# Kernel tuning notes

Hardware: AMD Instinct MI355X
Metric: run time of the kernel (lower is better)

The kernel has to match this reference:

```python
import jax, jax.numpy as jnp
import numpy as np

B, N, DIM, HEADS, NBS = 64, 197, 768, 12, 10
WIN = (14, 14)
HEAD_DIM = DIM // HEADS
SCALE = HEAD_DIM ** -0.5


def _gen_relative_position_index():
    Wh, Ww = WIN
    num_rel = (2 * Wh - 1) * (2 * Ww - 1) + 3
    coords = np.stack(np.meshgrid(np.arange(Wh), np.arange(Ww), indexing='ij')).reshape(2, -1)
    rel = (coords[:, :, None] - coords[:, None, :]).transpose(1, 2, 0).astype(np.int32)
    rel[:, :, 0] += Wh - 1
    rel[:, :, 1] += Ww - 1
    rel[:, :, 0] *= 2 * Ww - 1
    idx = np.zeros((Wh * Ww + 1, Wh * Ww + 1), dtype=np.int32)
    idx[1:, 1:] = rel.sum(-1)
    idx[0, :] = num_rel - 3
    idx[:, 0] = num_rel - 2
    idx[0, 0] = num_rel - 1
    return jnp.asarray(idx)


def setup_inputs() -> dict:
    key = jax.random.key(0)
    ks = jax.random.split(key, 8)
    s = 0.02  # init scale for learned params
    return {
        'x': jax.random.normal(ks[0], (B, N, DIM), jnp.float32),
        'qkv_weight': jax.random.normal(ks[1], (3 * DIM, DIM), jnp.float32) * s,
        'q_bias': jax.random.normal(ks[2], (NBS, DIM), jnp.float32) * s,
        'v_bias': jax.random.normal(ks[3], (NBS, DIM), jnp.float32) * s,
        'rel_table': jax.random.normal(ks[4], (732, HEADS), jnp.float32) * s,
        'proj_weight': jax.random.normal(ks[5], (DIM, DIM), jnp.float32) * s,
        'proj_bias': jax.random.normal(ks[6], (NBS, DIM), jnp.float32) * s,
        'b_idx': jax.random.randint(ks[7], (B,), 0, NBS),
        'rel_index': _gen_relative_position_index(),
    }


def reference(x, qkv_weight, q_bias, v_bias, rel_table, proj_weight, proj_bias, b_idx, rel_index):
    Bb, Nn, C = x.shape
    # QKV projection (no fused bias), then per-sample bitfit bias (k bias is zero)
    qkv = jnp.einsum('bnc,oc->bno', x, qkv_weight)  # [B, N, 3C]
    qb = q_bias[b_idx][:, None]                     # [B, 1, C]
    vb = v_bias[b_idx][:, None]
    qkv_bias = jnp.concatenate([qb, jnp.zeros_like(qb), vb], axis=-1)
    qkv = (qkv + qkv_bias).reshape(Bb, Nn, 3, HEADS, HEAD_DIM).transpose(2, 0, 3, 1, 4)
    q, k, v = qkv[0], qkv[1], qkv[2]                # [B, H, N, d]
    attn = jnp.einsum('bhnd,bhmd->bhnm', q * SCALE, k)
    # gathered relative position bias: [H, N, N]
    rel_bias = rel_table[rel_index.reshape(-1)].reshape(Nn, Nn, HEADS).transpose(2, 0, 1)
    attn = jax.nn.softmax(attn + rel_bias[None], axis=-1)
    out = jnp.einsum('bhnm,bhmd->bhnd', attn, v)
    out = out.transpose(0, 2, 1, 3).reshape(Bb, Nn, -1)
    # output projection with per-sample bitfit bias
    out = jnp.einsum('bnc,oc->bno', out, proj_weight) + proj_bias[b_idx][:, None]
    return out
```

## Files before the change

kernel.cpp:

```cpp
#include <hip/hip_runtime.h>
#include <stdint.h>

#define B_     64
#define N_     197
#define DIM_   768
#define HEADS_ 12
#define HD_    64
#define M_     (B_*N_)
#define K3_    (3*DIM_)
#define NP_    208
#define VSTR_  232
#define SCALE_ 0.125f
#define GK_    768
#define NKT_   24

typedef _Float16 f16x8 __attribute__((ext_vector_type(8)));
typedef _Float16 f16x4 __attribute__((ext_vector_type(4)));
typedef _Float16 f16x2 __attribute__((ext_vector_type(2)));
typedef float    f32x4 __attribute__((ext_vector_type(4)));

__device__ __forceinline__ void gload_lds16(const void* g, void* l) {
    __builtin_amdgcn_global_load_lds(
        (const __attribute__((address_space(1))) uint32_t*)g,
        (__attribute__((address_space(3))) uint32_t*)l, 16, 0, 0);
}

__global__ __launch_bounds__(256) void cvt_f32_f16(const float* __restrict__ s,
                                                   _Float16* __restrict__ d, int n4) {
    int i = blockIdx.x * 256 + threadIdx.x;
    if (i < n4) {
        const float4 v = *(const float4*)(s + (size_t)i * 4);
        f16x4 o;
        o[0] = (_Float16)v.x; o[1] = (_Float16)v.y;
        o[2] = (_Float16)v.z; o[3] = (_Float16)v.w;
        *(f16x4*)(d + (size_t)i * 4) = o;
    }
}

__global__ __launch_bounds__(256) void biasT_pre(const int* __restrict__ rel_index,
                                                 const float* __restrict__ rel_table,
                                                 float* __restrict__ biasT) {
    int t = blockIdx.x * 256 + threadIdx.x;
    if (t < HEADS_ * NP_ * NP_) {
        int h = t / (NP_ * NP_), rem = t - h * (NP_ * NP_);
        int k = rem / NP_, q = rem - k * NP_;
        float v;
        if (k >= N_)      v = -1e30f;
        else if (q >= N_) v = 0.f;
        else              v = rel_table[rel_index[q * N_ + k] * HEADS_ + h];
        biasT[t] = v;
    }
}

template <int MODE>
__global__ __launch_bounds__(512, 2) void gemm_db(
    const _Float16* __restrict__ A, const _Float16* __restrict__ Bw,
    int M, int Nout,
    const float* __restrict__ qb, const float* __restrict__ vb,
    const float* __restrict__ pb, const int* __restrict__ b_idx,
    _Float16* __restrict__ out_h, float* __restrict__ out_f)
{
    __shared__ __align__(16) _Float16 As[3][16 * 512];
    __shared__ __align__(16) _Float16 Bs[3][8 * 512];

    const int tid  = threadIdx.x;
    const int lane = tid & 63, w = tid >> 6;
    const int wm = w >> 1, wn = w & 1;
    const int fr = lane & 15, g = lane >> 4;
    const int gl8 = ((4 * fr + g) ^ (fr >> 1)) * 8;
    const int lx = lane ^ (lane >> 3);
    const int sr = lx >> 2, sc8 = (lx & 3) * 8;

    const int gx = Nout / 128;
    const int gy = (M + 255) / 256;
    const int nwg = gx * gy;
    const int wgid = blockIdx.x + blockIdx.y * gx;
    const int q8 = nwg >> 3, r8 = nwg & 7;
    const int xcd = wgid & 7, lid = wgid >> 3;
    const int nid = (xcd < r8) ? xcd * (q8 + 1) + lid
                               : r8 * (q8 + 1) + (xcd - r8) * q8 + lid;
    const int m0 = (nid / gx) * 256, n0 = (nid % gx) * 128;

    f32x4 acc[4][4];
    #pragma unroll
    for (int i = 0; i < 4; ++i)
        #pragma unroll
        for (int j = 0; j < 4; ++j) acc[i][j] = (f32x4)0.f;

    auto stage = [&](int buf, int kt) {
        #pragma unroll
        for (int iss = 0; iss < 2; ++iss) {
            int grow = m0 + w * 32 + iss * 16 + sr;
            if (grow >= M) grow = M - 1;
            gload_lds16(A + (size_t)grow * GK_ + kt * 32 + sc8,
                        &As[buf][(2 * w + iss) * 512]);
        }
        int brow = n0 + w * 16 + sr;
        gload_lds16(Bw + (size_t)brow * GK_ + kt * 32 + sc8,
                    &Bs[buf][w * 512]);
    };

    stage(0, 0);
    stage(1, 1);

    for (int t = 0; t < NKT_; ++t) {
        if (t + 1 < NKT_) { asm volatile("s_waitcnt vmcnt(3)" ::: "memory"); }
        else              { asm volatile("s_waitcnt vmcnt(0)" ::: "memory"); }
        __builtin_amdgcn_s_barrier();
        __builtin_amdgcn_sched_barrier(0);
        if (t + 2 < NKT_) stage((t + 2) % 3, t + 2);

        const _Float16* Ac = &As[t % 3][0];
        const _Float16* Bc = &Bs[t % 3][0];
        f16x8 av[4], bv[4];
        #pragma unroll
        for (int i = 0; i < 4; ++i)
            av[i] = *(const f16x8*)&Ac[(wm * 4 + i) * 512 + gl8];
        #pragma unroll
        for (int j = 0; j < 4; ++j)
            bv[j] = *(const f16x8*)&Bc[(wn * 4 + j) * 512 + gl8];
        __builtin_amdgcn_s_setprio(1);
        #pragma unroll
        for (int i = 0; i < 4; ++i)
            #pragma unroll
            for (int j = 0; j < 4; ++j)
                acc[i][j] = __builtin_amdgcn_mfma_f32_16x16x32_f16(av[i], bv[j], acc[i][j], 0, 0, 0);
        __builtin_amdgcn_s_setprio(0);
    }

    #pragma unroll
    for (int mi = 0; mi < 4; ++mi) {
        #pragma unroll
        for (int rr = 0; rr < 4; ++rr) {
            const int row = m0 + wm * 64 + mi * 16 + g * 4 + rr;
            if (row < M) {
                const int bi = b_idx[row / N_];
                #pragma unroll
                for (int ni = 0; ni < 4; ++ni) {
                    const int col = n0 + wn * 64 + ni * 16 + fr;
                    float v = acc[mi][ni][rr];
                    if (MODE == 0) {
                        float bias = 0.f;
                        if (col < DIM_) bias = qb[bi * DIM_ + col];
                        else if (col >= 2 * DIM_) bias = vb[bi * DIM_ + (col - 2 * DIM_)];
                        out_h[(size_t)row * Nout + col] = (_Float16)(v + bias);
                    } else {
                        out_f[(size_t)row * Nout + col] = v + pb[bi * DIM_ + col];
                    }
                }
            }
        }
    }
}

__global__ __launch_bounds__(512, 4) void attn_mfma(
    const _Float16* __restrict__ qkv, const float* __restrict__ biasT,
    _Float16* __restrict__ ctx)
{
    __shared__ __align__(16) _Float16 Klds[26 * 512];
    __shared__ __align__(16) _Float16 VT[HD_ * VSTR_];

    const int b = blockIdx.z, h = blockIdx.y, rt = blockIdx.x;
    const int r0 = rt * 128;
    const int tid = threadIdx.x, lane = tid & 63, w = tid >> 6;
    const int fr = lane & 15, g = lane >> 4;
    const int gl8 = ((4 * fr + g) ^ (fr >> 1)) * 8;

    const size_t baseQ = (size_t)b * N_ * K3_ + h * HD_;
    const size_t baseK = baseQ + DIM_;
    const size_t baseV = baseQ + 2 * DIM_;

    {
        const int l = lane ^ (lane >> 3);
        const int cr = l >> 2, cc = (l & 3) * 8;
        for (int c = w; c < 26; c += 8) {
            const int jf = c >> 1, kk = c & 1;
            int grow = jf * 16 + cr; if (grow > N_ - 1) grow = N_ - 1;
            gload_lds16(qkv + baseK + (size_t)grow * K3_ + kk * 32 + cc,
                        &Klds[c * 512]);
        }
    }
    for (int idx = tid; idx < 112 * 8; idx += 512) {
        int jp = idx % 112, dc = idx / 112;
        int j0 = 2 * jp, j1 = 2 * jp + 1;
        f16x8 zz = {};
        f16x8 v0 = (j0 < N_) ? *(const f16x8*)(qkv + baseV + (size_t)j0 * K3_ + dc * 8) : zz;
        f16x8 v1 = (j1 < N_) ? *(const f16x8*)(qkv + baseV + (size_t)j1 * K3_ + dc * 8) : zz;
        #pragma unroll
        for (int e = 0; e < 8; ++e) {
            f16x2 p; p[0] = v0[e]; p[1] = v1[e];
            *(f16x2*)(VT + (dc * 8 + e) * VSTR_ + 2 * jp) = p;
        }
    }
    int qrow = r0 + w * 16 + fr; if (qrow > N_ - 1) qrow = N_ - 1;
    f16x8 qf[2];
    qf[0] = *(const f16x8*)(qkv + baseQ + (size_t)qrow * K3_ + g * 8);
    qf[1] = *(const f16x8*)(qkv + baseQ + (size_t)qrow * K3_ + 32 + g * 8);

    __syncthreads();

    f32x4 p[13];
    #pragma unroll
    for (int jf = 0; jf < 13; ++jf) p[jf] = (f32x4)0.f;
    #pragma unroll
    for (int jf = 0; jf < 13; ++jf) {
        #pragma unroll
        for (int kk = 0; kk < 2; ++kk) {
            f16x8 a = *(const f16x8*)&Klds[(jf * 2 + kk) * 512 + gl8];
            p[jf] = __builtin_amdgcn_mfma_f32_16x16x32_f16(a, qf[kk], p[jf], 0, 0, 0);
        }
    }

    const int qb_ = min(r0 + w * 16 + fr, NP_ - 1);
    const float* bp = biasT + (size_t)h * NP_ * NP_ + qb_;
    float mx = -3e38f;
    #pragma unroll
    for (int jf = 0; jf < 13; ++jf) {
        #pragma unroll
        for (int r = 0; r < 4; ++r) {
            int k = jf * 16 + g * 4 + r;
            float s = p[jf][r] * SCALE_ + bp[(size_t)k * NP_];
            p[jf][r] = s;
            mx = fmaxf(mx, s);
        }
    }
    mx = fmaxf(mx, __shfl_xor(mx, 16));
    mx = fmaxf(mx, __shfl_xor(mx, 32));
    float sum = 0.f;
    #pragma unroll
    for (int jf = 0; jf < 13; ++jf) {
        #pragma unroll
        for (int r = 0; r < 4; ++r) {
            float e = __expf(p[jf][r] - mx);
            p[jf][r] = e;
            sum += e;
        }
    }
    sum += __shfl_xor(sum, 16);
    sum += __shfl_xor(sum, 32);
    const float inv = 1.f / sum;

    const int src0 = ((2 * g) & 3) * 16 + fr;
    const int src1 = ((2 * g + 1) & 3) * 16 + fr;
    const bool hi = (g >= 2);
    f32x4 oacc[4];
    #pragma unroll
    for (int dj = 0; dj < 4; ++dj) oacc[dj] = (f32x4)0.f;

    #pragma unroll
    for (int ks = 0; ks < 7; ++ks) {
        f16x2 t;
        t[0] = (_Float16)(p[2 * ks][0] * inv); t[1] = (_Float16)(p[2 * ks][1] * inv);
        uint32_t a01 = __builtin_bit_cast(uint32_t, t);
        t[0] = (_Float16)(p[2 * ks][2] * inv); t[1] = (_Float16)(p[2 * ks][3] * inv);
        uint32_t a23 = __builtin_bit_cast(uint32_t, t);
        uint32_t b01 = 0, b23 = 0;
        if (ks < 6) {
            t[0] = (_Float16)(p[2 * ks + 1][0] * inv); t[1] = (_Float16)(p[2 * ks + 1][1] * inv);
            b01 = __builtin_bit_cast(uint32_t, t);
            t[0] = (_Float16)(p[2 * ks + 1][2] * inv); t[1] = (_Float16)(p[2 * ks + 1][3] * inv);
            b23 = __builtin_bit_cast(uint32_t, t);
        }
        uint32_t xa, xb;
        uint32_t wd[4];
        xa = (uint32_t)__shfl((int)a01, src0); xb = (uint32_t)__shfl((int)b01, src0);
        wd[0] = hi ? xb : xa;
        xa = (uint32_t)__shfl((int)a23, src0); xb = (uint32_t)__shfl((int)b23, src0);
        wd[1] = hi ? xb : xa;
        xa = (uint32_t)__shfl((int)a01, src1); xb = (uint32_t)__shfl((int)b01, src1);
        wd[2] = hi ? xb : xa;
        xa = (uint32_t)__shfl((int)a23, src1); xb = (uint32_t)__shfl((int)b23, src1);
        wd[3] = hi ? xb : xa;
        typedef uint32_t u32x4 __attribute__((ext_vector_type(4)));
        u32x4 wv; wv[0] = wd[0]; wv[1] = wd[1]; wv[2] = wd[2]; wv[3] = wd[3];
        f16x8 af = __builtin_bit_cast(f16x8, wv);

        #pragma unroll
        for (int dj = 0; dj < 4; ++dj) {
            f16x8 bf = *(const f16x8*)&VT[(dj * 16 + fr) * VSTR_ + ks * 32 + g * 8];
            oacc[dj] = __builtin_amdgcn_mfma_f32_16x16x32_f16(af, bf, oacc[dj], 0, 0, 0);
        }
    }

    #pragma unroll
    for (int dj = 0; dj < 4; ++dj) {
        #pragma unroll
        for (int r = 0; r < 4; ++r) {
            const int q = r0 + w * 16 + g * 4 + r;
            if (q < N_)
                ctx[((size_t)b * N_ + q) * DIM_ + h * HD_ + dj * 16 + fr] =
                    (_Float16)oacc[dj][r];
        }
    }
}

extern "C" void kernel_launch(void* const* d_in, const int* in_sizes, int n_in,
                              void* d_out, int out_size, void* d_ws, size_t ws_size,
                              hipStream_t stream) {
    const float* x     = (const float*)d_in[0];
    const float* wqkv  = (const float*)d_in[1];
    const float* qb    = (const float*)d_in[2];
    const float* vb    = (const float*)d_in[3];
    const float* rt    = (const float*)d_in[4];
    const float* wproj = (const float*)d_in[5];
    const float* pbias = (const float*)d_in[6];
    const int* b_idx   = (const int*)d_in[7];
    const int* rel_idx = (const int*)d_in[8];
    float* out = (float*)d_out;

    char* ws = (char*)d_ws;
    size_t off = 0;
    auto alloc = [&](size_t bytes) -> void* {
        void* p = ws + off; off += (bytes + 255) & ~(size_t)255; return p;
    };
    _Float16* xb    = (_Float16*)alloc((size_t)M_ * DIM_ * 2);
    _Float16* wqh   = (_Float16*)alloc((size_t)K3_ * DIM_ * 2);
    _Float16* wph   = (_Float16*)alloc((size_t)DIM_ * DIM_ * 2);
    _Float16* qkvh  = (_Float16*)alloc((size_t)M_ * K3_ * 2);
    _Float16* ctx   = (_Float16*)alloc((size_t)M_ * DIM_ * 2);
    float*    biasT = (float*)alloc((size_t)HEADS_ * NP_ * NP_ * 4);

    cvt_f32_f16<<<dim3((M_ * DIM_ / 4 + 255) / 256), 256, 0, stream>>>(x, xb, M_ * DIM_ / 4);
    cvt_f32_f16<<<dim3((K3_ * DIM_ / 4 + 255) / 256), 256, 0, stream>>>(wqkv, wqh, K3_ * DIM_ / 4);
    cvt_f32_f16<<<dim3((DIM_ * DIM_ / 4 + 255) / 256), 256, 0, stream>>>(wproj, wph, DIM_ * DIM_ / 4);
    biasT_pre<<<dim3((HEADS_ * NP_ * NP_ + 255) / 256), 256, 0, stream>>>(rel_idx, rt, biasT);

    gemm_db<0><<<dim3(K3_ / 128, (M_ + 255) / 256), 512, 0, stream>>>(
        xb, wqh, M_, K3_, qb, vb, nullptr, b_idx, qkvh, nullptr);

    attn_mfma<<<dim3(2, HEADS_, B_), 512, 0, stream>>>(qkvh, biasT, ctx);

    gemm_db<1><<<dim3(DIM_ / 128, (M_ + 255) / 256), 512, 0, stream>>>(
        ctx, wph, M_, DIM_, nullptr, nullptr, pbias, b_idx, nullptr, out);
}
```

Measured before the change: 169.7 us.

## Fuse x fp32-to-fp16 conversion into QKV GEMM and merge prep kernels

The QKV GEMM now loads fp32 activations straight into LDS with a swizzled layout and converts them to fp16 while building MFMA fragments. This removes the separate x conversion kernel and its fp16 round trip through memory. The weight conversions and the bias table build are merged into one grid-stride prep kernel, cutting launches. In exchange, the GEMM moves twice the A bytes per tile, drops from a triple-buffered to a double-buffered pipeline with a full vmcnt(0) wait each step, and adds conversion ALU work in the inner loop.

```diff
diff --git a/kernel.cpp b/kernel.cpp
--- a/kernel.cpp
+++ b/kernel.cpp
@@ -25,40 +25,151 @@
         (__attribute__((address_space(3))) uint32_t*)l, 16, 0, 0);
 }
 
-__global__ __launch_bounds__(256) void cvt_f32_f16(const float* __restrict__ s,
-                                                   _Float16* __restrict__ d, int n4) {
-    int i = blockIdx.x * 256 + threadIdx.x;
-    if (i < n4) {
-        const float4 v = *(const float4*)(s + (size_t)i * 4);
-        f16x4 o;
-        o[0] = (_Float16)v.x; o[1] = (_Float16)v.y;
-        o[2] = (_Float16)v.z; o[3] = (_Float16)v.w;
-        *(f16x4*)(d + (size_t)i * 4) = o;
-    }
-}
-
-__global__ __launch_bounds__(256) void biasT_pre(const int* __restrict__ rel_index,
-                                                 const float* __restrict__ rel_table,
-                                                 float* __restrict__ biasT) {
-    int t = blockIdx.x * 256 + threadIdx.x;
-    if (t < HEADS_ * NP_ * NP_) {
-        int h = t / (NP_ * NP_), rem = t - h * (NP_ * NP_);
-        int k = rem / NP_, q = rem - k * NP_;
-        float v;
-        if (k >= N_)      v = -1e30f;
-        else if (q >= N_) v = 0.f;
-        else              v = rel_table[rel_index[q * N_ + k] * HEADS_ + h];
-        biasT[t] = v;
-    }
-}
-
-template <int MODE>
-__global__ __launch_bounds__(512, 2) void gemm_db(
+#define PW0_ (K3_*DIM_/8)
+#define PW1_ (DIM_*DIM_/8)
+#define PW2_ (HEADS_*NP_*NP_)
+__global__ __launch_bounds__(256) void prep(
+    const float* __restrict__ wqkv, const float* __restrict__ wproj,
+    const int* __restrict__ rel_index, const float* __restrict__ rel_table,
+    _Float16* __restrict__ wqh, _Float16* __restrict__ wph,
+    float* __restrict__ biasT)
+{
+    const int stride = gridDim.x * 256;
+    for (int i = blockIdx.x * 256 + threadIdx.x; i < PW0_ + PW1_ + PW2_; i += stride) {
+        if (i < PW0_) {
+            const float4 v0 = *(const float4*)(wqkv + (size_t)i * 8);
+            const float4 v1 = *(const float4*)(wqkv + (size_t)i * 8 + 4);
+            f16x8 o;
+            o[0]=(_Float16)v0.x; o[1]=(_Float16)v0.y; o[2]=(_Float16)v0.z; o[3]=(_Float16)v0.w;
+            o[4]=(_Float16)v1.x; o[5]=(_Float16)v1.y; o[6]=(_Float16)v1.z; o[7]=(_Float16)v1.w;
+            *(f16x8*)(wqh + (size_t)i * 8) = o;
+        } else if (i < PW0_ + PW1_) {
+            const int j = i - PW0_;
+            const float4 v0 = *(const float4*)(wproj + (size_t)j * 8);
+            const float4 v1 = *(const float4*)(wproj + (size_t)j * 8 + 4);
+            f16x8 o;
+            o[0]=(_Float16)v0.x; o[1]=(_Float16)v0.y; o[2]=(_Float16)v0.z; o[3]=(_Float16)v0.w;
+            o[4]=(_Float16)v1.x; o[5]=(_Float16)v1.y; o[6]=(_Float16)v1.z; o[7]=(_Float16)v1.w;
+            *(f16x8*)(wph + (size_t)j * 8) = o;
+        } else {
+            const int t = i - PW0_ - PW1_;
+            const int h = t / (NP_ * NP_), rem = t - h * (NP_ * NP_);
+            const int k = rem / NP_, q = rem - k * NP_;
+            float v;
+            if (k >= N_)      v = -1e30f;
+            else if (q >= N_) v = 0.f;
+            else              v = rel_table[rel_index[q * N_ + k] * HEADS_ + h];
+            biasT[t] = v;
+        }
+    }
+}
+
+__global__ __launch_bounds__(512, 2) void gemm_qkv(
+    const float* __restrict__ X, const _Float16* __restrict__ Bw,
+    const float* __restrict__ qb, const float* __restrict__ vb,
+    const int* __restrict__ b_idx, _Float16* __restrict__ out_h)
+{
+    __shared__ __align__(16) float    Af[2][32 * 256];
+    __shared__ __align__(16) _Float16 Bs[2][8 * 512];
+
+    const int tid  = threadIdx.x;
+    const int lane = tid & 63, w = tid >> 6;
+    const int wm = w >> 1, wn = w & 1;
+    const int fr = lane & 15, g = lane >> 4;
+    const int gl8 = ((4 * fr + g) ^ (fr >> 1)) * 8;
+    const int lx = lane ^ (lane >> 3);
+    const int srB = lx >> 2, scB = (lx & 3) * 8;
+    const int lr = lane >> 3, lc = lane & 7;
+
+    const int gx = K3_ / 128, gy = (M_ + 255) / 256;
+    const int nwg = gx * gy;
+    const int wgid = blockIdx.x + blockIdx.y * gx;
+    const int q8 = nwg >> 3, r8 = nwg & 7;
+    const int xcd = wgid & 7, lid = wgid >> 3;
+    const int nid = (xcd < r8) ? xcd * (q8 + 1) + lid
+                               : r8 * (q8 + 1) + (xcd - r8) * q8 + lid;
+    const int m0 = (nid / gx) * 256, n0 = (nid % gx) * 128;
+
+    f32x4 acc[4][4];
+    #pragma unroll
+    for (int i = 0; i < 4; ++i)
+        #pragma unroll
+        for (int j = 0; j < 4; ++j) acc[i][j] = (f32x4)0.f;
+
+    auto stage = [&](int buf, int kt) {
+        #pragma unroll
+        for (int q = 0; q < 4; ++q) {
+            const int c = w * 4 + q;
+            int grow = m0 + c * 8 + lr;
+            if (grow >= M_) grow = M_ - 1;
+            const int gcol = kt * 32 + ((lc ^ lr ^ (c & 7)) * 4);
+            gload_lds16(X + (size_t)grow * GK_ + gcol, &Af[buf][c * 256]);
+        }
+        const int brow = n0 + w * 16 + srB;
+        gload_lds16(Bw + (size_t)brow * GK_ + kt * 32 + scB, &Bs[buf][w * 512]);
+    };
+
+    stage(0, 0);
+    asm volatile("s_waitcnt vmcnt(0)" ::: "memory");
+    __builtin_amdgcn_s_barrier();
+
+    for (int t = 0; t < NKT_; ++t) {
+        const int cur = t & 1;
+        if (t + 1 < NKT_) stage(cur ^ 1, t + 1);
+
+        f16x8 av[4], bv[4];
+        #pragma unroll
+        for (int i = 0; i < 4; ++i) {
+            const int R = wm * 64 + i * 16 + fr;
+            const int C = R >> 3, r = R & 7;
+            const float* base = &Af[cur][C * 256 + r * 32];
+            f32x4 lo = *(const f32x4*)&base[(((2 * g)     ^ r ^ (C & 7)) * 4)];
+            f32x4 hi = *(const f32x4*)&base[(((2 * g + 1) ^ r ^ (C & 7)) * 4)];
+            f16x8 o;
+            o[0]=(_Float16)lo[0]; o[1]=(_Float16)lo[1]; o[2]=(_Float16)lo[2]; o[3]=(_Float16)lo[3];
+            o[4]=(_Float16)hi[0]; o[5]=(_Float16)hi[1]; o[6]=(_Float16)hi[2]; o[7]=(_Float16)hi[3];
+            av[i] = o;
+        }
+        #pragma unroll
+        for (int j = 0; j < 4; ++j)
+            bv[j] = *(const f16x8*)&Bs[cur][(wn * 4 + j) * 512 + gl8];
+        __builtin_amdgcn_s_setprio(1);
+        #pragma unroll
+        for (int i = 0; i < 4; ++i)
+            #pragma unroll
+            for (int j = 0; j < 4; ++j)
+                acc[i][j] = __builtin_amdgcn_mfma_f32_16x16x32_f16(av[i], bv[j], acc[i][j], 0, 0, 0);
+        __builtin_amdgcn_s_setprio(0);
+        if (t + 1 < NKT_) {
+            asm volatile("s_waitcnt vmcnt(0)" ::: "memory");
+            __builtin_amdgcn_s_barrier();
+        }
+    }
+
+    #pragma unroll
+    for (int mi = 0; mi < 4; ++mi) {
+        #pragma unroll
+        for (int rr = 0; rr < 4; ++rr) {
+            const int row = m0 + wm * 64 + mi * 16 + g * 4 + rr;
+            if (row < M_) {
+                const int bi = b_idx[row / N_];
+                #pragma unroll
+                for (int ni = 0; ni < 4; ++ni) {
+                    const int col = n0 + wn * 64 + ni * 16 + fr;
+                    float bias = 0.f;
+                    if (col < DIM_) bias = qb[bi * DIM_ + col];
+                    else if (col >= 2 * DIM_) bias = vb[bi * DIM_ + (col - 2 * DIM_)];
+                    out_h[(size_t)row * K3_ + col] = (_Float16)(acc[mi][ni][rr] + bias);
+                }
+            }
+        }
+    }
+}
+
+__global__ __launch_bounds__(512, 2) void gemm_proj(
     const _Float16* __restrict__ A, const _Float16* __restrict__ Bw,
-    int M, int Nout,
-    const float* __restrict__ qb, const float* __restrict__ vb,
     const float* __restrict__ pb, const int* __restrict__ b_idx,
-    _Float16* __restrict__ out_h, float* __restrict__ out_f)
+    float* __restrict__ out_f)
 {
     __shared__ __align__(16) _Float16 As[3][16 * 512];
     __shared__ __align__(16) _Float16 Bs[3][8 * 512];
@@ -71,8 +182,7 @@
     const int lx = lane ^ (lane >> 3);
     const int sr = lx >> 2, sc8 = (lx & 3) * 8;
 
-    const int gx = Nout / 128;
-    const int gy = (M + 255) / 256;
+    const int gx = DIM_ / 128, gy = (M_ + 255) / 256;
     const int nwg = gx * gy;
     const int wgid = blockIdx.x + blockIdx.y * gx;
     const int q8 = nwg >> 3, r8 = nwg & 7;
@@ -91,7 +201,7 @@
         #pragma unroll
         for (int iss = 0; iss < 2; ++iss) {
             int grow = m0 + w * 32 + iss * 16 + sr;
-            if (grow >= M) grow = M - 1;
+            if (grow >= M_) grow = M_ - 1;
             gload_lds16(A + (size_t)grow * GK_ + kt * 32 + sc8,
                         &As[buf][(2 * w + iss) * 512]);
         }
@@ -133,20 +243,12 @@
         #pragma unroll
         for (int rr = 0; rr < 4; ++rr) {
             const int row = m0 + wm * 64 + mi * 16 + g * 4 + rr;
-            if (row < M) {
+            if (row < M_) {
                 const int bi = b_idx[row / N_];
                 #pragma unroll
                 for (int ni = 0; ni < 4; ++ni) {
                     const int col = n0 + wn * 64 + ni * 16 + fr;
-                    float v = acc[mi][ni][rr];
-                    if (MODE == 0) {
-                        float bias = 0.f;
-                        if (col < DIM_) bias = qb[bi * DIM_ + col];
-                        else if (col >= 2 * DIM_) bias = vb[bi * DIM_ + (col - 2 * DIM_)];
-                        out_h[(size_t)row * Nout + col] = (_Float16)(v + bias);
-                    } else {
-                        out_f[(size_t)row * Nout + col] = v + pb[bi * DIM_ + col];
-                    }
+                    out_f[(size_t)row * DIM_ + col] = acc[mi][ni][rr] + pb[bi * DIM_ + col];
                 }
             }
         }
@@ -313,23 +415,19 @@
     auto alloc = [&](size_t bytes) -> void* {
         void* p = ws + off; off += (bytes + 255) & ~(size_t)255; return p;
     };
-    _Float16* xb    = (_Float16*)alloc((size_t)M_ * DIM_ * 2);
     _Float16* wqh   = (_Float16*)alloc((size_t)K3_ * DIM_ * 2);
     _Float16* wph   = (_Float16*)alloc((size_t)DIM_ * DIM_ * 2);
     _Float16* qkvh  = (_Float16*)alloc((size_t)M_ * K3_ * 2);
     _Float16* ctx   = (_Float16*)alloc((size_t)M_ * DIM_ * 2);
     float*    biasT = (float*)alloc((size_t)HEADS_ * NP_ * NP_ * 4);
 
-    cvt_f32_f16<<<dim3((M_ * DIM_ / 4 + 255) / 256), 256, 0, stream>>>(x, xb, M_ * DIM_ / 4);
-    cvt_f32_f16<<<dim3((K3_ * DIM_ / 4 + 255) / 256), 256, 0, stream>>>(wqkv, wqh, K3_ * DIM_ / 4);
-    cvt_f32_f16<<<dim3((DIM_ * DIM_ / 4 + 255) / 256), 256, 0, stream>>>(wproj, wph, DIM_ * DIM_ / 4);
-    biasT_pre<<<dim3((HEADS_ * NP_ * NP_ + 255) / 256), 256, 0, stream>>>(rel_idx, rt, biasT);
-
-    gemm_db<0><<<dim3(K3_ / 128, (M_ + 255) / 256), 512, 0, stream>>>(
-        xb, wqh, M_, K3_, qb, vb, nullptr, b_idx, qkvh, nullptr);
+    prep<<<dim3(1024), 256, 0, stream>>>(wqkv, wproj, rel_idx, rt, wqh, wph, biasT);
+
+    gemm_qkv<<<dim3(K3_ / 128, (M_ + 255) / 256), 512, 0, stream>>>(
+        x, wqh, qb, vb, b_idx, qkvh);
 
     attn_mfma<<<dim3(2, HEADS_, B_), 512, 0, stream>>>(qkvh, biasT, ctx);
 
-    gemm_db<1><<<dim3(DIM_ / 128, (M_ + 255) / 256), 512, 0, stream>>>(
-        ctx, wph, M_, DIM_, nullptr, nullptr, pbias, b_idx, nullptr, out);
-}
+    gemm_proj<<<dim3(DIM_ / 128, (M_ + 255) / 256), 512, 0, stream>>>(
+        ctx, wph, pbias, b_idx, out);
+}
```

New measurement: 226.3 us. +33.3%, slower.
